# Kernel optimization log

Measured on AMD Instinct MI355X. Metric: run time of the kernel, lower is better.

Reference implementation:

```python
import jax, jax.numpy as jnp
import numpy as np

N_NODES = 256  # num_eeg_channels; reshape in head forces node count == channels

def setup_inputs() -> dict:
    key = jax.random.key(0)
    ks = jax.random.split(key, 16)
    T, H, L, E = 30000, 512, 256, 32768
    def w(k, shape):
        return jax.random.normal(k, shape, jnp.float32) / np.sqrt(shape[0]).astype(np.float32)
    return {
        "eeg_nodes": jax.random.normal(ks[0], (N_NODES, T), jnp.float32),
        "eeg_idx": jax.random.randint(ks[1], (2, E), 0, N_NODES),
        "eeg_attr": jax.random.uniform(ks[2], (E,), jnp.float32),
        # struct_featurizer GIN: conv1 MLP [T,H,H], conv2 MLP [H,L,L]
        "Ws1a": w(ks[3], (T, H)), "bs1a": jnp.zeros((H,), jnp.float32),
        "Ws1b": w(ks[4], (H, H)), "bs1b": jnp.zeros((H,), jnp.float32),
        "Ws2a": w(ks[5], (H, L)), "bs2a": jnp.zeros((L,), jnp.float32),
        "Ws2b": w(ks[6], (L, L)), "bs2b": jnp.zeros((L,), jnp.float32),
        # gin_scorer GIN: conv1 MLP [L,H,H], conv2 MLP [H,1,1]
        "Wc1a": w(ks[7], (L, H)), "bc1a": jnp.zeros((H,), jnp.float32),
        "Wc1b": w(ks[8], (H, H)), "bc1b": jnp.zeros((H,), jnp.float32),
        "Wc2a": w(ks[9], (H, 1)), "bc2a": jnp.zeros((1,), jnp.float32),
        "Wc2b": w(ks[10], (1, 1)), "bc2b": jnp.zeros((1,), jnp.float32),
        # dementia head: Linear(N*L, 1)
        "Wd": w(ks[11], (N_NODES * L, 1)), "bd": jnp.zeros((1,), jnp.float32),
    }


def _gin_conv(x, src, dst, W1, b1, W2, b2):
    # GINConv, eps=0: nn(x + sum_{j in N(i)} x_j); edge weights unsupported/ignored.
    agg = jax.ops.segment_sum(x[src], dst, num_segments=N_NODES)
    h = x + agg
    h = jax.nn.relu(h @ W1 + b1)  # MLP([in, out, out]) = Linear-ReLU-Linear
    return h @ W2 + b2


def reference(eeg_nodes, eeg_idx, eeg_attr,
              Ws1a, bs1a, Ws1b, bs1b, Ws2a, bs2a, Ws2b, bs2b,
              Wc1a, bc1a, Wc1b, bc1b, Wc2a, bc2a, Wc2b, bc2b,
              Wd, bd):
    src, dst = eeg_idx[0], eeg_idx[1]
    # struct_featurizer (2-layer GIN; inter-layer ReLU, edge_weight ignored by GINConv)
    h = _gin_conv(eeg_nodes, src, dst, Ws1a, bs1a, Ws1b, bs1b)
    h = jax.nn.relu(h)
    feat = _gin_conv(h, src, dst, Ws2a, bs2a, Ws2b, bs2b)  # [N, L]
    # gin_scorer (2-layer GIN)
    s = _gin_conv(feat, src, dst, Wc1a, bc1a, Wc1b, bc1b)
    s = jax.nn.relu(s)
    s = _gin_conv(s, src, dst, Wc2a, bc2a, Wc2b, bc2b)  # [N, 1]
    region_scores = jax.nn.sigmoid(s)
    flat = feat.reshape(1, -1)  # [1, N*L]
    dementia_pred = jax.nn.sigmoid(flat @ Wd + bd)  # [1, 1]
    return dementia_pred, region_scores
```

## Files before the change

### kernel.cpp

```cpp
#include <hip/hip_runtime.h>
#include <math.h>

#define N_NODES 256
#define T_DIM   30000
#define T_PAD   30016
#define H_DIM   512
#define L_DIM   256

typedef __attribute__((ext_vector_type(8))) short short8;
typedef __attribute__((ext_vector_type(4))) float floatx4;

__global__ void k_init_P(float* P, float* dem, float* u) {
    int t = blockIdx.x * blockDim.x + threadIdx.x;
    P[t] = ((t >> 8) == (t & 255)) ? 1.0f : 0.0f;
    if (t == 0) *dem = 0.0f;
    if (t < 256) u[t] = 0.0f;
}

__global__ void k_count_edges(const int* __restrict__ idx, int E, float* P) {
    int e = blockIdx.x * blockDim.x + threadIdx.x;
    if (e < E) {
        int s = idx[e];
        int d = idx[E + e];
        atomicAdd(&P[d * N_NODES + s], 1.0f);
    }
}

__global__ void k_zero(float* p, int n) {
    int t = blockIdx.x * blockDim.x + threadIdx.x;
    if (t < n) p[t] = 0.0f;
}

__device__ __forceinline__ unsigned short f2b(float f) {
    unsigned u = __float_as_uint(f);
    u += 0x7fffu + ((u >> 16) & 1u);
    return (unsigned short)(u >> 16);
}

__device__ __forceinline__ float4 zero4() {
    float4 z; z.x = z.y = z.z = z.w = 0.f; return z;
}

__global__ __launch_bounds__(256)
void k_gemm_mfma(const float* __restrict__ x, const float* __restrict__ W,
                 float* __restrict__ outp, int kc) {
    __shared__ unsigned short Al[128 * 40];
    __shared__ unsigned short Bl[128 * 40];

    const int t = threadIdx.x;
    const int orig = blockIdx.x;
    const int q = gridDim.x >> 3;
    const int L = (orig & 7) * q + (orig >> 3);
    const int tile = L & 7;
    const int colBase = (tile & 3) << 7;
    const int rowBase = (tile >> 2) << 7;
    const int z = L >> 3;
    const int kb0 = z * kc;
    const int kend = min(kb0 + kc, T_PAD);
    const int nchunk = (kend - kb0) >> 5;

    const int s_row  = t >> 1;
    const int s_half = (t & 1) << 4;
    const int s_k  = t & 31;
    const int s_cq = (t >> 5) << 4;

    const int w    = t >> 6;
    const int wr   = (w >> 1) << 6;
    const int wc   = (w & 1) << 6;
    const int lane = t & 63;
    const int lm   = lane & 15;
    const int lq   = (lane >> 4) << 3;

    floatx4 acc[4][4];
    #pragma unroll
    for (int i = 0; i < 4; ++i)
        #pragma unroll
        for (int j = 0; j < 4; ++j)
            acc[i][j] = (floatx4){0.f, 0.f, 0.f, 0.f};

    float4 pa[4], pb[4];
    {
        const int kg = kb0;
        const float* ap = x + (size_t)(rowBase + s_row) * T_DIM + kg + s_half;
        #pragma unroll
        for (int i = 0; i < 4; ++i)
            pa[i] = (kg + s_half + i * 4 + 4 <= T_DIM) ? *(const float4*)(ap + i * 4)
                                                       : zero4();
        const float* bp = W + (size_t)(kg + s_k) * H_DIM + colBase + s_cq;
        #pragma unroll
        for (int i = 0; i < 4; ++i)
            pb[i] = (kg + s_k < T_DIM) ? *(const float4*)(bp + i * 4) : zero4();
    }

    #pragma unroll 1
    for (int c = 0; c < nchunk; ++c) {
        __syncthreads();
        #pragma unroll
        for (int i = 0; i < 4; ++i) {
            ushort4 uv;
            uv.x = f2b(pa[i].x); uv.y = f2b(pa[i].y);
            uv.z = f2b(pa[i].z); uv.w = f2b(pa[i].w);
            *(ushort4*)&Al[s_row * 40 + s_half + i * 4] = uv;
        }
        #pragma unroll
        for (int i = 0; i < 4; ++i) {
            const int cb = s_cq + i * 4;
            Bl[(cb + 0) * 40 + s_k] = f2b(pb[i].x);
            Bl[(cb + 1) * 40 + s_k] = f2b(pb[i].y);
            Bl[(cb + 2) * 40 + s_k] = f2b(pb[i].z);
            Bl[(cb + 3) * 40 + s_k] = f2b(pb[i].w);
        }
        __syncthreads();

        if (c + 1 < nchunk) {
            const int kg = kb0 + (c + 1) * 32;
            const float* ap = x + (size_t)(rowBase + s_row) * T_DIM + kg + s_half;
            #pragma unroll
            for (int i = 0; i < 4; ++i)
                pa[i] = (kg + s_half + i * 4 + 4 <= T_DIM)
                            ? *(const float4*)(ap + i * 4) : zero4();
            const float* bp = W + (size_t)(kg + s_k) * H_DIM + colBase + s_cq;
            #pragma unroll
            for (int i = 0; i < 4; ++i)
                pb[i] = (kg + s_k < T_DIM) ? *(const float4*)(bp + i * 4) : zero4();
        }

        short8 af[4], bf[4];
        #pragma unroll
        for (int i = 0; i < 4; ++i)
            af[i] = *(const short8*)&Al[(wr + i * 16 + lm) * 40 + lq];
        #pragma unroll
        for (int j = 0; j < 4; ++j)
            bf[j] = *(const short8*)&Bl[(wc + j * 16 + lm) * 40 + lq];
        #pragma unroll
        for (int i = 0; i < 4; ++i)
            #pragma unroll
            for (int j = 0; j < 4; ++j)
                acc[i][j] = __builtin_amdgcn_mfma_f32_16x16x32_bf16(
                    af[i], bf[j], acc[i][j], 0, 0, 0);
    }

    float* op = outp + (size_t)z * (N_NODES * H_DIM);
    const int rq = (lane >> 4) << 2;
    #pragma unroll
    for (int i = 0; i < 4; ++i) {
        #pragma unroll
        for (int j = 0; j < 4; ++j) {
            const int r  = rowBase + wr + i * 16 + rq;
            const int cc = colBase + wc + j * 16 + lm;
            op[(size_t)(r + 0) * H_DIM + cc] = acc[i][j][0];
            op[(size_t)(r + 1) * H_DIM + cc] = acc[i][j][1];
            op[(size_t)(r + 2) * H_DIM + cc] = acc[i][j][2];
            op[(size_t)(r + 3) * H_DIM + cc] = acc[i][j][3];
        }
    }
}

__global__ __launch_bounds__(256)
void k_gemm_big_atomic(const float* __restrict__ x, const float* __restrict__ W,
                       float* __restrict__ outp, int kc) {
    __shared__ float xs[16 * 140];
    __shared__ float ws[16 * 132];
    const int t  = threadIdx.x;
    const int colBase = blockIdx.x * 128;
    const int rowBase = blockIdx.y * 128;
    const int kb0  = blockIdx.z * kc;
    const int kend = min(kb0 + kc, T_DIM);
    const int nchunk = (kend > kb0) ? ((kend - kb0) >> 4) : 0;
    const int lr  = t >> 2, lkq = (t & 3) * 4;
    const int wkk = t >> 5, wcq = (t & 31) * 4;
    const int tx  = t & 15, ty = t >> 4;
    float acc[8][8];
    #pragma unroll
    for (int i = 0; i < 8; ++i)
        #pragma unroll
        for (int j = 0; j < 8; ++j) acc[i][j] = 0.0f;
    #pragma unroll 1
    for (int c = 0; c < nchunk; ++c) {
        int kb = kb0 + c * 16;
        __syncthreads();
        const float* xp = x + (size_t)(rowBase + lr) * T_DIM + kb + lkq;
        float4 xa = *(const float4*)xp;
        float4 xb = *(const float4*)(xp + (size_t)64 * T_DIM);
        const float* wp = W + (size_t)(kb + wkk) * H_DIM + colBase + wcq;
        float4 wa = *(const float4*)wp;
        float4 wb = *(const float4*)(wp + 8 * H_DIM);
        xs[(lkq + 0) * 140 + lr] = xa.x; xs[(lkq + 1) * 140 + lr] = xa.y;
        xs[(lkq + 2) * 140 + lr] = xa.z; xs[(lkq + 3) * 140 + lr] = xa.w;
        xs[(lkq + 0) * 140 + lr + 64] = xb.x; xs[(lkq + 1) * 140 + lr + 64] = xb.y;
        xs[(lkq + 2) * 140 + lr + 64] = xb.z; xs[(lkq + 3) * 140 + lr + 64] = xb.w;
        *(float4*)&ws[wkk * 132 + wcq]       = wa;
        *(float4*)&ws[(wkk + 8) * 132 + wcq] = wb;
        __syncthreads();
        #pragma unroll
        for (int kk = 0; kk < 16; ++kk) {
            float a[8], b[8];
            *(float4*)&a[0] = *(const float4*)&xs[kk * 140 + ty * 8];
            *(float4*)&a[4] = *(const float4*)&xs[kk * 140 + ty * 8 + 4];
            *(float4*)&b[0] = *(const float4*)&ws[kk * 132 + tx * 8];
            *(float4*)&b[4] = *(const float4*)&ws[kk * 132 + tx * 8 + 4];
            #pragma unroll
            for (int i = 0; i < 8; ++i)
                #pragma unroll
                for (int j = 0; j < 8; ++j)
                    acc[i][j] = fmaf(a[i], b[j], acc[i][j]);
        }
    }
    if (nchunk == 0) return;
    #pragma unroll
    for (int i = 0; i < 8; ++i) {
        int r = rowBase + ty * 8 + i;
        #pragma unroll
        for (int j = 0; j < 8; ++j)
            atomicAdd(&outp[r * H_DIM + colBase + tx * 8 + j], acc[i][j]);
    }
}

__global__ void k_reduce(const float2* __restrict__ Y1p, float2* __restrict__ Y1,
                         int nz) {
    int i = blockIdx.x * blockDim.x + threadIdx.x;
    float2 s = Y1p[i];
    for (int z = 1; z < nz; ++z) {
        float2 v = Y1p[(size_t)z * 65536 + i];
        s.x += v.x; s.y += v.y;
    }
    Y1[i] = s;
}

template<int K, int N, int MODE>
__global__ __launch_bounds__(256)
void k_mstage(const float* __restrict__ A, const float* __restrict__ B,
              const float* __restrict__ bias, float* __restrict__ out, int act,
              const float* __restrict__ Wd, float* __restrict__ dem,
              const float* __restrict__ uW, float* __restrict__ u) {
    const int t = threadIdx.x;
    const int wv = (blockIdx.x << 2) | (t >> 6);
    const int nct = N >> 4;
    const int r0 = (wv / nct) << 4;
    const int c0 = (wv % nct) << 4;
    const int lane = t & 63;
    const int lm   = lane & 15;
    const int lq   = (lane >> 4) << 3;

    floatx4 accE = {0.f, 0.f, 0.f, 0.f};
    floatx4 accO = {0.f, 0.f, 0.f, 0.f};
    const float* ap = A + (size_t)(r0 + lm) * K + lq;
    const float* bp = B + (size_t)lq * N + c0 + lm;

    #pragma unroll 2
    for (int kb = 0; kb < K; kb += 64) {
        {
            float4 a0 = *(const float4*)(ap + kb);
            float4 a1 = *(const float4*)(ap + kb + 4);
            float b0 = bp[(size_t)(kb + 0) * N], b1 = bp[(size_t)(kb + 1) * N];
            float b2 = bp[(size_t)(kb + 2) * N], b3 = bp[(size_t)(kb + 3) * N];
            float b4 = bp[(size_t)(kb + 4) * N], b5 = bp[(size_t)(kb + 5) * N];
            float b6 = bp[(size_t)(kb + 6) * N], b7 = bp[(size_t)(kb + 7) * N];
            short8 af, bf;
            af[0] = (short)f2b(a0.x); af[1] = (short)f2b(a0.y);
            af[2] = (short)f2b(a0.z); af[3] = (short)f2b(a0.w);
            af[4] = (short)f2b(a1.x); af[5] = (short)f2b(a1.y);
            af[6] = (short)f2b(a1.z); af[7] = (short)f2b(a1.w);
            bf[0] = (short)f2b(b0); bf[1] = (short)f2b(b1);
            bf[2] = (short)f2b(b2); bf[3] = (short)f2b(b3);
            bf[4] = (short)f2b(b4); bf[5] = (short)f2b(b5);
            bf[6] = (short)f2b(b6); bf[7] = (short)f2b(b7);
            accE = __builtin_amdgcn_mfma_f32_16x16x32_bf16(af, bf, accE, 0, 0, 0);
        }
        {
            const int kc2 = kb + 32;
            float4 a0 = *(const float4*)(ap + kc2);
            float4 a1 = *(const float4*)(ap + kc2 + 4);
            float b0 = bp[(size_t)(kc2 + 0) * N], b1 = bp[(size_t)(kc2 + 1) * N];
            float b2 = bp[(size_t)(kc2 + 2) * N], b3 = bp[(size_t)(kc2 + 3) * N];
            float b4 = bp[(size_t)(kc2 + 4) * N], b5 = bp[(size_t)(kc2 + 5) * N];
            float b6 = bp[(size_t)(kc2 + 6) * N], b7 = bp[(size_t)(kc2 + 7) * N];
            short8 af, bf;
            af[0] = (short)f2b(a0.x); af[1] = (short)f2b(a0.y);
            af[2] = (short)f2b(a0.z); af[3] = (short)f2b(a0.w);
            af[4] = (short)f2b(a1.x); af[5] = (short)f2b(a1.y);
            af[6] = (short)f2b(a1.z); af[7] = (short)f2b(a1.w);
            bf[0] = (short)f2b(b0); bf[1] = (short)f2b(b1);
            bf[2] = (short)f2b(b2); bf[3] = (short)f2b(b3);
            bf[4] = (short)f2b(b4); bf[5] = (short)f2b(b5);
            bf[6] = (short)f2b(b6); bf[7] = (short)f2b(b7);
            accO = __builtin_amdgcn_mfma_f32_16x16x32_bf16(af, bf, accO, 0, 0, 0);
        }
    }

    const float bb = bias ? bias[c0 + lm] : 0.f;
    const int rq = (lane >> 4) << 2;
    float v[4];
    #pragma unroll
    for (int i = 0; i < 4; ++i) {
        v[i] = accE[i] + accO[i] + bb;
        if (act) v[i] = fmaxf(v[i], 0.f);
    }

    if (MODE == 2) {
        const float uw = uW[c0 + lm];
        #pragma unroll
        for (int i = 0; i < 4; ++i) {
            float p = v[i] * uw;
            #pragma unroll
            for (int off = 8; off; off >>= 1) p += __shfl_down(p, off, 16);
            if (lm == 0) atomicAdd(&u[r0 + rq + i], p);
        }
        return;
    }
    #pragma unroll
    for (int i = 0; i < 4; ++i)
        out[(size_t)(r0 + rq + i) * N + c0 + lm] = v[i];
    if (MODE == 1) {
        float p = 0.f;
        #pragma unroll
        for (int i = 0; i < 4; ++i)
            p += v[i] * Wd[(r0 + rq + i) * 256 + c0 + lm];
        #pragma unroll
        for (int off = 32; off; off >>= 1) p += __shfl_down(p, off, 64);
        if (lane == 0) atomicAdd(dem, p);
    }
}

__device__ __forceinline__ float sigmoidf(float x) {
    return 1.0f / (1.0f + expf(-x));
}

__global__ __launch_bounds__(256)
void k_final(const float* __restrict__ P, const float* __restrict__ u,
             const float* __restrict__ dem,
             const float* __restrict__ bc2a, const float* __restrict__ Wc2b,
             const float* __restrict__ bc2b, const float* __restrict__ bd,
             float* __restrict__ out) {
    __shared__ float red[4];
    const int b = blockIdx.x, t = threadIdx.x;
    float pv = P[b * 256 + t] * u[t];
    #pragma unroll
    for (int off = 32; off; off >>= 1) pv += __shfl_down(pv, off, 64);
    if ((t & 63) == 0) red[t >> 6] = pv;
    __syncthreads();
    if (t == 0) {
        float v = red[0] + red[1] + red[2] + red[3];
        float h2 = fmaxf(v + bc2a[0], 0.f);
        out[1 + b] = sigmoidf(h2 * Wc2b[0] + bc2b[0]);
        if (b == 0) out[0] = sigmoidf(*dem + bd[0]);
    }
}

extern "C" void kernel_launch(void* const* d_in, const int* in_sizes, int n_in,
                              void* d_out, int out_size, void* d_ws, size_t ws_size,
                              hipStream_t stream) {
    const float* x    = (const float*)d_in[0];
    const int*   idx  = (const int*)d_in[1];
    const float* Ws1a = (const float*)d_in[3];
    const float* bs1a = (const float*)d_in[4];
    const float* Ws1b = (const float*)d_in[5];
    const float* bs1b = (const float*)d_in[6];
    const float* Ws2a = (const float*)d_in[7];
    const float* bs2a = (const float*)d_in[8];
    const float* Ws2b = (const float*)d_in[9];
    const float* bs2b = (const float*)d_in[10];
    const float* Wc1a = (const float*)d_in[11];
    const float* bc1a = (const float*)d_in[12];
    const float* Wc1b = (const float*)d_in[13];
    const float* bc1b = (const float*)d_in[14];
    const float* Wc2a = (const float*)d_in[15];
    const float* bc2a = (const float*)d_in[16];
    const float* Wc2b = (const float*)d_in[17];
    const float* bc2b = (const float*)d_in[18];
    const float* Wd   = (const float*)d_in[19];
    const float* bd   = (const float*)d_in[20];
    float* out = (float*)d_out;
    const int E = in_sizes[1] / 2;

    float* w    = (float*)d_ws;
    float* P    = w;
    float* Y1   = P + 65536;
    float* bufA = Y1 + 131072;
    float* bufB = bufA + 131072;
    float* feat = bufB + 131072;
    float* u    = feat + 65536;
    float* dem  = u + 256;
    float* Y1p  = dem + 64;

    const long long fixed = (long long)(Y1p - w);
    const long long avail = (long long)(ws_size / 4) - fixed;
    int maxsplit = (avail > 0) ? (int)(avail / 131072) : 0;
    int nz = 0, kc = 0;
    const int CH32 = 938;
    if (maxsplit >= 2) {
        int splits = maxsplit < 56 ? maxsplit : 56;
        int cps = (CH32 + splits - 1) / splits;
        nz = (CH32 + cps - 1) / cps;
        kc = cps * 32;
    }

    k_init_P<<<256, 256, 0, stream>>>(P, dem, u);
    k_count_edges<<<(E + 255) / 256, 256, 0, stream>>>(idx, E, P);

    if (nz > 0) {
        k_gemm_mfma<<<8 * nz, 256, 0, stream>>>(x, Ws1a, Y1p, kc);
        k_reduce<<<256, 256, 0, stream>>>((const float2*)Y1p, (float2*)Y1, nz);
    } else {
        k_zero<<<512, 256, 0, stream>>>(Y1, N_NODES * H_DIM);
        k_gemm_big_atomic<<<dim3(4, 2, 63), 256, 0, stream>>>(x, Ws1a, Y1, 480);
    }

    k_mstage<256, 512, 0><<<128, 256, 0, stream>>>(P,    Y1,   bs1a, bufA, 1, 0, 0, 0, 0);
    k_mstage<512, 512, 0><<<128, 256, 0, stream>>>(bufA, Ws1b, bs1b, bufB, 1, 0, 0, 0, 0);
    k_mstage<256, 512, 0><<<128, 256, 0, stream>>>(P,    bufB, 0,    bufA, 0, 0, 0, 0, 0);
    k_mstage<512, 256, 0><<< 64, 256, 0, stream>>>(bufA, Ws2a, bs2a, bufB, 1, 0, 0, 0, 0);
    k_mstage<256, 256, 1><<< 64, 256, 0, stream>>>(bufB, Ws2b, bs2b, feat, 0, Wd, dem, 0, 0);
    k_mstage<256, 256, 0><<< 64, 256, 0, stream>>>(P,    feat, 0,    bufA, 0, 0, 0, 0, 0);
    k_mstage<256, 512, 0><<<128, 256, 0, stream>>>(bufA, Wc1a, bc1a, bufB, 1, 0, 0, 0, 0);
    k_mstage<512, 512, 2><<<128, 256, 0, stream>>>(bufB, Wc1b, bc1b, 0,    1, 0, 0, Wc2a, u);
    k_final<<<256, 256, 0, stream>>>(P, u, dem, bc2a, Wc2b, bc2b, bd, out);
}
```

Measured before the change: 267.7 us.

## Fuse post-GEMM stages into one cooperative kernel with grid syncs

Replaces the init, edge-count, reduce, eight matmul-stage and final launches with a single cooperative kernel of 512 one-wave blocks. Stages are separated by grid.sync instead of kernel boundaries, so per-launch overhead and idle gaps between small kernels go away. Stage code is moved into a shared device function with runtime K/N/MODE and no loop unrolling, which may cost some instruction efficiency. If the cooperative launch fails, the code falls back to the original multi-kernel sequence.

```diff
diff --git a/kernel.cpp b/kernel.cpp
--- a/kernel.cpp
+++ b/kernel.cpp
@@ -1,5 +1,8 @@
 #include <hip/hip_runtime.h>
+#include <hip/hip_cooperative_groups.h>
 #include <math.h>
+
+namespace cg = cooperative_groups;
 
 #define N_NODES 256
 #define T_DIM   30000
@@ -227,35 +230,31 @@
     Y1[i] = s;
 }
 
-template<int K, int N, int MODE>
-__global__ __launch_bounds__(256)
-void k_mstage(const float* __restrict__ A, const float* __restrict__ B,
-              const float* __restrict__ bias, float* __restrict__ out, int act,
-              const float* __restrict__ Wd, float* __restrict__ dem,
-              const float* __restrict__ uW, float* __restrict__ u) {
-    const int t = threadIdx.x;
-    const int wv = (blockIdx.x << 2) | (t >> 6);
+__device__ __forceinline__ void wave_stage(
+    int tile, int K, int N, int MODE,
+    const float* __restrict__ A, const float* __restrict__ B,
+    const float* __restrict__ bias, float* __restrict__ outp, int act,
+    const float* __restrict__ Wd, float* __restrict__ dem,
+    const float* __restrict__ uW, float* __restrict__ u, int lane) {
     const int nct = N >> 4;
-    const int r0 = (wv / nct) << 4;
-    const int c0 = (wv % nct) << 4;
-    const int lane = t & 63;
-    const int lm   = lane & 15;
-    const int lq   = (lane >> 4) << 3;
+    const int r0 = (tile / nct) << 4;
+    const int c0 = (tile % nct) << 4;
+    const int lm = lane & 15;
+    const int lq = (lane >> 4) << 3;
 
     floatx4 accE = {0.f, 0.f, 0.f, 0.f};
     floatx4 accO = {0.f, 0.f, 0.f, 0.f};
     const float* ap = A + (size_t)(r0 + lm) * K + lq;
     const float* bp = B + (size_t)lq * N + c0 + lm;
 
-    #pragma unroll 2
+    #pragma unroll 1
     for (int kb = 0; kb < K; kb += 64) {
         {
             float4 a0 = *(const float4*)(ap + kb);
             float4 a1 = *(const float4*)(ap + kb + 4);
-            float b0 = bp[(size_t)(kb + 0) * N], b1 = bp[(size_t)(kb + 1) * N];
-            float b2 = bp[(size_t)(kb + 2) * N], b3 = bp[(size_t)(kb + 3) * N];
-            float b4 = bp[(size_t)(kb + 4) * N], b5 = bp[(size_t)(kb + 5) * N];
-            float b6 = bp[(size_t)(kb + 6) * N], b7 = bp[(size_t)(kb + 7) * N];
+            const float* bq = bp + (size_t)kb * N;
+            float b0 = bq[0],     b1 = bq[(size_t)N],     b2 = bq[(size_t)2*N], b3 = bq[(size_t)3*N];
+            float b4 = bq[(size_t)4*N], b5 = bq[(size_t)5*N], b6 = bq[(size_t)6*N], b7 = bq[(size_t)7*N];
             short8 af, bf;
             af[0] = (short)f2b(a0.x); af[1] = (short)f2b(a0.y);
             af[2] = (short)f2b(a0.z); af[3] = (short)f2b(a0.w);
@@ -268,13 +267,12 @@
             accE = __builtin_amdgcn_mfma_f32_16x16x32_bf16(af, bf, accE, 0, 0, 0);
         }
         {
-            const int kc2 = kb + 32;
-            float4 a0 = *(const float4*)(ap + kc2);
-            float4 a1 = *(const float4*)(ap + kc2 + 4);
-            float b0 = bp[(size_t)(kc2 + 0) * N], b1 = bp[(size_t)(kc2 + 1) * N];
-            float b2 = bp[(size_t)(kc2 + 2) * N], b3 = bp[(size_t)(kc2 + 3) * N];
-            float b4 = bp[(size_t)(kc2 + 4) * N], b5 = bp[(size_t)(kc2 + 5) * N];
-            float b6 = bp[(size_t)(kc2 + 6) * N], b7 = bp[(size_t)(kc2 + 7) * N];
+            const int k2 = kb + 32;
+            float4 a0 = *(const float4*)(ap + k2);
+            float4 a1 = *(const float4*)(ap + k2 + 4);
+            const float* bq = bp + (size_t)k2 * N;
+            float b0 = bq[0],     b1 = bq[(size_t)N],     b2 = bq[(size_t)2*N], b3 = bq[(size_t)3*N];
+            float b4 = bq[(size_t)4*N], b5 = bq[(size_t)5*N], b6 = bq[(size_t)6*N], b7 = bq[(size_t)7*N];
             short8 af, bf;
             af[0] = (short)f2b(a0.x); af[1] = (short)f2b(a0.y);
             af[2] = (short)f2b(a0.z); af[3] = (short)f2b(a0.w);
@@ -310,7 +308,7 @@
     }
     #pragma unroll
     for (int i = 0; i < 4; ++i)
-        out[(size_t)(r0 + rq + i) * N + c0 + lm] = v[i];
+        outp[(size_t)(r0 + rq + i) * N + c0 + lm] = v[i];
     if (MODE == 1) {
         float p = 0.f;
         #pragma unroll
@@ -320,6 +318,17 @@
         for (int off = 32; off; off >>= 1) p += __shfl_down(p, off, 64);
         if (lane == 0) atomicAdd(dem, p);
     }
+}
+
+template<int K, int N, int MODE>
+__global__ __launch_bounds__(256)
+void k_mstage(const float* __restrict__ A, const float* __restrict__ B,
+              const float* __restrict__ bias, float* __restrict__ out, int act,
+              const float* __restrict__ Wd, float* __restrict__ dem,
+              const float* __restrict__ uW, float* __restrict__ u) {
+    const int t = threadIdx.x;
+    const int wv = (blockIdx.x << 2) | (t >> 6);
+    wave_stage(wv, K, N, MODE, A, B, bias, out, act, Wd, dem, uW, u, t & 63);
 }
 
 __device__ __forceinline__ float sigmoidf(float x) {
@@ -344,6 +353,84 @@
         float h2 = fmaxf(v + bc2a[0], 0.f);
         out[1 + b] = sigmoidf(h2 * Wc2b[0] + bc2b[0]);
         if (b == 0) out[0] = sigmoidf(*dem + bd[0]);
+    }
+}
+
+__global__ __launch_bounds__(64)
+void k_fused(const int* __restrict__ idx, int E, int nz,
+             const float* __restrict__ Y1p, float* __restrict__ Y1,
+             float* __restrict__ P,
+             const float* __restrict__ bs1a, const float* __restrict__ Ws1b,
+             const float* __restrict__ bs1b, const float* __restrict__ Ws2a,
+             const float* __restrict__ bs2a, const float* __restrict__ Ws2b,
+             const float* __restrict__ bs2b, const float* __restrict__ Wc1a,
+             const float* __restrict__ bc1a, const float* __restrict__ Wc1b,
+             const float* __restrict__ bc1b, const float* __restrict__ Wc2a,
+             const float* __restrict__ bc2a, const float* __restrict__ Wc2b,
+             const float* __restrict__ bc2b, const float* __restrict__ Wd,
+             const float* __restrict__ bd,
+             float* __restrict__ bufA, float* __restrict__ bufB,
+             float* __restrict__ feat, float* __restrict__ u,
+             float* __restrict__ dem, float* __restrict__ out) {
+    cg::grid_group grid = cg::this_grid();
+    const int b = blockIdx.x;
+    const int lane = threadIdx.x;
+    const int gid = (b << 6) | lane;
+
+    #pragma unroll
+    for (int i = gid; i < 65536; i += 32768)
+        P[i] = ((i >> 8) == (i & 255)) ? 1.0f : 0.0f;
+    if (nz > 0) {
+        const float4* src = (const float4*)Y1p;
+        float4 s = src[gid];
+        for (int z = 1; z < nz; ++z) {
+            float4 v = src[(size_t)z * 32768 + gid];
+            s.x += v.x; s.y += v.y; s.z += v.z; s.w += v.w;
+        }
+        ((float4*)Y1)[gid] = s;
+    }
+    if (gid < 256) u[gid] = 0.0f;
+    if (gid == 0) *dem = 0.0f;
+    grid.sync();
+
+    for (int e = gid; e < E; e += 32768) {
+        int s = idx[e];
+        int d = idx[E + e];
+        atomicAdd(&P[d * N_NODES + s], 1.0f);
+    }
+    grid.sync();
+
+    wave_stage(b, 256, 512, 0, P,    Y1,   bs1a, bufA, 1, 0, 0, 0, 0, lane);
+    grid.sync();
+    wave_stage(b, 512, 512, 0, bufA, Ws1b, bs1b, bufB, 1, 0, 0, 0, 0, lane);
+    grid.sync();
+    wave_stage(b, 256, 512, 0, P,    bufB, 0,    bufA, 0, 0, 0, 0, 0, lane);
+    grid.sync();
+    if (b < 256) wave_stage(b, 512, 256, 0, bufA, Ws2a, bs2a, bufB, 1, 0, 0, 0, 0, lane);
+    grid.sync();
+    if (b < 256) wave_stage(b, 256, 256, 1, bufB, Ws2b, bs2b, feat, 0, Wd, dem, 0, 0, lane);
+    grid.sync();
+    if (b < 256) wave_stage(b, 256, 256, 0, P,    feat, 0,    bufA, 0, 0, 0, 0, 0, lane);
+    grid.sync();
+    wave_stage(b, 256, 512, 0, bufA, Wc1a, bc1a, bufB, 1, 0, 0, 0, 0, lane);
+    grid.sync();
+    wave_stage(b, 512, 512, 2, bufB, Wc1b, bc1b, 0,    1, 0, 0, Wc2a, u, lane);
+    grid.sync();
+
+    if (b < 256) {
+        float pv = 0.f;
+        #pragma unroll
+        for (int j = 0; j < 4; ++j) {
+            int c = lane + 64 * j;
+            pv += P[b * 256 + c] * u[c];
+        }
+        #pragma unroll
+        for (int off = 32; off; off >>= 1) pv += __shfl_down(pv, off, 64);
+        if (lane == 0) {
+            float h2 = fmaxf(pv + bc2a[0], 0.f);
+            out[1 + b] = sigmoidf(h2 * Wc2b[0] + bc2b[0]);
+            if (b == 0) out[0] = sigmoidf(*dem + bd[0]);
+        }
     }
 }
 
@@ -371,7 +458,7 @@
     const float* Wd   = (const float*)d_in[19];
     const float* bd   = (const float*)d_in[20];
     float* out = (float*)d_out;
-    const int E = in_sizes[1] / 2;
+    int E = in_sizes[1] / 2;
 
     float* w    = (float*)d_ws;
     float* P    = w;
@@ -395,24 +482,36 @@
         kc = cps * 32;
     }
 
-    k_init_P<<<256, 256, 0, stream>>>(P, dem, u);
-    k_count_edges<<<(E + 255) / 256, 256, 0, stream>>>(idx, E, P);
-
     if (nz > 0) {
         k_gemm_mfma<<<8 * nz, 256, 0, stream>>>(x, Ws1a, Y1p, kc);
-        k_reduce<<<256, 256, 0, stream>>>((const float2*)Y1p, (float2*)Y1, nz);
     } else {
         k_zero<<<512, 256, 0, stream>>>(Y1, N_NODES * H_DIM);
         k_gemm_big_atomic<<<dim3(4, 2, 63), 256, 0, stream>>>(x, Ws1a, Y1, 480);
     }
 
-    k_mstage<256, 512, 0><<<128, 256, 0, stream>>>(P,    Y1,   bs1a, bufA, 1, 0, 0, 0, 0);
-    k_mstage<512, 512, 0><<<128, 256, 0, stream>>>(bufA, Ws1b, bs1b, bufB, 1, 0, 0, 0, 0);
-    k_mstage<256, 512, 0><<<128, 256, 0, stream>>>(P,    bufB, 0,    bufA, 0, 0, 0, 0, 0);
-    k_mstage<512, 256, 0><<< 64, 256, 0, stream>>>(bufA, Ws2a, bs2a, bufB, 1, 0, 0, 0, 0);
-    k_mstage<256, 256, 1><<< 64, 256, 0, stream>>>(bufB, Ws2b, bs2b, feat, 0, Wd, dem, 0, 0);
-    k_mstage<256, 256, 0><<< 64, 256, 0, stream>>>(P,    feat, 0,    bufA, 0, 0, 0, 0, 0);
-    k_mstage<256, 512, 0><<<128, 256, 0, stream>>>(bufA, Wc1a, bc1a, bufB, 1, 0, 0, 0, 0);
-    k_mstage<512, 512, 2><<<128, 256, 0, stream>>>(bufB, Wc1b, bc1b, 0,    1, 0, 0, Wc2a, u);
-    k_final<<<256, 256, 0, stream>>>(P, u, dem, bc2a, Wc2b, bc2b, bd, out);
-}
+    void* args[] = {
+        (void*)&idx, (void*)&E, (void*)&nz, (void*)&Y1p, (void*)&Y1, (void*)&P,
+        (void*)&bs1a, (void*)&Ws1b, (void*)&bs1b, (void*)&Ws2a, (void*)&bs2a,
+        (void*)&Ws2b, (void*)&bs2b, (void*)&Wc1a, (void*)&bc1a, (void*)&Wc1b,
+        (void*)&bc1b, (void*)&Wc2a, (void*)&bc2a, (void*)&Wc2b, (void*)&bc2b,
+        (void*)&Wd, (void*)&bd, (void*)&bufA, (void*)&bufB, (void*)&feat,
+        (void*)&u, (void*)&dem, (void*)&out
+    };
+    hipError_t ce = hipLaunchCooperativeKernel((const void*)k_fused, dim3(512),
+                                               dim3(64), args, 0, stream);
+    if (ce != hipSuccess) {
+        k_init_P<<<256, 256, 0, stream>>>(P, dem, u);
+        k_count_edges<<<(E + 255) / 256, 256, 0, stream>>>(idx, E, P);
+        if (nz > 0)
+            k_reduce<<<256, 256, 0, stream>>>((const float2*)Y1p, (float2*)Y1, nz);
+        k_mstage<256, 512, 0><<<128, 256, 0, stream>>>(P,    Y1,   bs1a, bufA, 1, 0, 0, 0, 0);
+        k_mstage<512, 512, 0><<<128, 256, 0, stream>>>(bufA, Ws1b, bs1b, bufB, 1, 0, 0, 0, 0);
+        k_mstage<256, 512, 0><<<128, 256, 0, stream>>>(P,    bufB, 0,    bufA, 0, 0, 0, 0, 0);
+        k_mstage<512, 256, 0><<< 64, 256, 0, stream>>>(bufA, Ws2a, bs2a, bufB, 1, 0, 0, 0, 0);
+        k_mstage<256, 256, 1><<< 64, 256, 0, stream>>>(bufB, Ws2b, bs2b, feat, 0, Wd, dem, 0, 0);
+        k_mstage<256, 256, 0><<< 64, 256, 0, stream>>>(P,    feat, 0,    bufA, 0, 0, 0, 0, 0);
+        k_mstage<256, 512, 0><<<128, 256, 0, stream>>>(bufA, Wc1a, bc1a, bufB, 1, 0, 0, 0, 0);
+        k_mstage<512, 512, 2><<<128, 256, 0, stream>>>(bufB, Wc1b, bc1b, 0,    1, 0, 0, Wc2a, u);
+        k_final<<<256, 256, 0, stream>>>(P, u, dem, bc2a, Wc2b, bc2b, bd, out);
+    }
+}
```

Result: slower. 798.6 us (+198.3%).

## Double-buffer global prefetch in big GEMM and fuse adjacency build into one kernel

Applied to the files above, without the earlier changes.

The main split-K MFMA GEMM now keeps two register sets of prefetched tiles and loads chunk c+2 while computing chunk c, which deepens the global-load pipeline to hide more latency at the cost of extra registers. Building the adjacency matrix now takes one kernel instead of init plus atomic edge counting: each block scans all edges and counts its own row in shared-memory atomics. This removes a launch and global atomics but makes each of the 256 blocks read the full edge list. The small MFMA stage gets a minor rewrite of its B-pointer arithmetic.

```diff
diff --git a/kernel.cpp b/kernel.cpp
--- a/kernel.cpp
+++ b/kernel.cpp
@@ -10,19 +10,21 @@
 typedef __attribute__((ext_vector_type(8))) short short8;
 typedef __attribute__((ext_vector_type(4))) float floatx4;
 
-__global__ void k_init_P(float* P, float* dem, float* u) {
-    int t = blockIdx.x * blockDim.x + threadIdx.x;
-    P[t] = ((t >> 8) == (t & 255)) ? 1.0f : 0.0f;
-    if (t == 0) *dem = 0.0f;
-    if (t < 256) u[t] = 0.0f;
-}
-
-__global__ void k_count_edges(const int* __restrict__ idx, int E, float* P) {
-    int e = blockIdx.x * blockDim.x + threadIdx.x;
-    if (e < E) {
-        int s = idx[e];
-        int d = idx[E + e];
-        atomicAdd(&P[d * N_NODES + s], 1.0f);
+__global__ __launch_bounds__(256)
+void k_buildP(const int* __restrict__ idx, int E, float* __restrict__ P,
+              float* __restrict__ dem, float* __restrict__ u) {
+    __shared__ float cnt[256];
+    const int row = blockIdx.x, t = threadIdx.x;
+    cnt[t] = 0.f;
+    __syncthreads();
+    for (int e = t; e < E; e += 256) {
+        if (idx[E + e] == row) atomicAdd(&cnt[idx[e]], 1.0f);
+    }
+    __syncthreads();
+    P[row * 256 + t] = cnt[t] + ((t == row) ? 1.0f : 0.0f);
+    if (row == 0) {
+        u[t] = 0.f;
+        if (t == 0) *dem = 0.f;
     }
 }
 
@@ -78,67 +80,66 @@
         for (int j = 0; j < 4; ++j)
             acc[i][j] = (floatx4){0.f, 0.f, 0.f, 0.f};
 
-    float4 pa[4], pb[4];
-    {
-        const int kg = kb0;
-        const float* ap = x + (size_t)(rowBase + s_row) * T_DIM + kg + s_half;
-        #pragma unroll
-        for (int i = 0; i < 4; ++i)
-            pa[i] = (kg + s_half + i * 4 + 4 <= T_DIM) ? *(const float4*)(ap + i * 4)
-                                                       : zero4();
-        const float* bp = W + (size_t)(kg + s_k) * H_DIM + colBase + s_cq;
-        #pragma unroll
-        for (int i = 0; i < 4; ++i)
-            pb[i] = (kg + s_k < T_DIM) ? *(const float4*)(bp + i * 4) : zero4();
-    }
+    float4 paA[4], pbA[4], paB[4], pbB[4];
+
+#define GLOAD(PA, PB, C) do {                                                  \
+        const int kg_ = kb0 + (C) * 32;                                        \
+        const float* ap_ = x + (size_t)(rowBase + s_row) * T_DIM + kg_ + s_half;\
+        _Pragma("unroll")                                                      \
+        for (int i_ = 0; i_ < 4; ++i_)                                         \
+            PA[i_] = (kg_ + s_half + i_ * 4 + 4 <= T_DIM)                      \
+                         ? *(const float4*)(ap_ + i_ * 4) : zero4();           \
+        const float* bp_ = W + (size_t)(kg_ + s_k) * H_DIM + colBase + s_cq;   \
+        _Pragma("unroll")                                                      \
+        for (int i_ = 0; i_ < 4; ++i_)                                         \
+            PB[i_] = (kg_ + s_k < T_DIM) ? *(const float4*)(bp_ + i_ * 4)      \
+                                         : zero4();                            \
+    } while (0)
+
+#define CHUNK_STEP(PA, PB, C) do {                                             \
+        __syncthreads();                                                       \
+        _Pragma("unroll")                                                      \
+        for (int i_ = 0; i_ < 4; ++i_) {                                       \
+            ushort4 uv_;                                                       \
+            uv_.x = f2b(PA[i_].x); uv_.y = f2b(PA[i_].y);                      \
+            uv_.z = f2b(PA[i_].z); uv_.w = f2b(PA[i_].w);                      \
+            *(ushort4*)&Al[s_row * 40 + s_half + i_ * 4] = uv_;                \
+        }                                                                      \
+        _Pragma("unroll")                                                      \
+        for (int i_ = 0; i_ < 4; ++i_) {                                       \
+            const int cb_ = s_cq + i_ * 4;                                     \
+            Bl[(cb_ + 0) * 40 + s_k] = f2b(PB[i_].x);                          \
+            Bl[(cb_ + 1) * 40 + s_k] = f2b(PB[i_].y);                          \
+            Bl[(cb_ + 2) * 40 + s_k] = f2b(PB[i_].z);                          \
+            Bl[(cb_ + 3) * 40 + s_k] = f2b(PB[i_].w);                          \
+        }                                                                      \
+        __syncthreads();                                                       \
+        if ((C) + 2 < nchunk) GLOAD(PA, PB, (C) + 2);                          \
+        short8 af_[4], bf_[4];                                                 \
+        _Pragma("unroll")                                                      \
+        for (int i_ = 0; i_ < 4; ++i_)                                         \
+            af_[i_] = *(const short8*)&Al[(wr + i_ * 16 + lm) * 40 + lq];      \
+        _Pragma("unroll")                                                      \
+        for (int j_ = 0; j_ < 4; ++j_)                                         \
+            bf_[j_] = *(const short8*)&Bl[(wc + j_ * 16 + lm) * 40 + lq];      \
+        _Pragma("unroll")                                                      \
+        for (int i_ = 0; i_ < 4; ++i_)                                         \
+            _Pragma("unroll")                                                  \
+            for (int j_ = 0; j_ < 4; ++j_)                                     \
+                acc[i_][j_] = __builtin_amdgcn_mfma_f32_16x16x32_bf16(         \
+                    af_[i_], bf_[j_], acc[i_][j_], 0, 0, 0);                   \
+    } while (0)
+
+    GLOAD(paA, pbA, 0);
+    if (nchunk > 1) GLOAD(paB, pbB, 1);
 
     #pragma unroll 1
-    for (int c = 0; c < nchunk; ++c) {
-        __syncthreads();
-        #pragma unroll
-        for (int i = 0; i < 4; ++i) {
-            ushort4 uv;
-            uv.x = f2b(pa[i].x); uv.y = f2b(pa[i].y);
-            uv.z = f2b(pa[i].z); uv.w = f2b(pa[i].w);
-            *(ushort4*)&Al[s_row * 40 + s_half + i * 4] = uv;
-        }
-        #pragma unroll
-        for (int i = 0; i < 4; ++i) {
-            const int cb = s_cq + i * 4;
-            Bl[(cb + 0) * 40 + s_k] = f2b(pb[i].x);
-            Bl[(cb + 1) * 40 + s_k] = f2b(pb[i].y);
-            Bl[(cb + 2) * 40 + s_k] = f2b(pb[i].z);
-            Bl[(cb + 3) * 40 + s_k] = f2b(pb[i].w);
-        }
-        __syncthreads();
-
-        if (c + 1 < nchunk) {
-            const int kg = kb0 + (c + 1) * 32;
-            const float* ap = x + (size_t)(rowBase + s_row) * T_DIM + kg + s_half;
-            #pragma unroll
-            for (int i = 0; i < 4; ++i)
-                pa[i] = (kg + s_half + i * 4 + 4 <= T_DIM)
-                            ? *(const float4*)(ap + i * 4) : zero4();
-            const float* bp = W + (size_t)(kg + s_k) * H_DIM + colBase + s_cq;
-            #pragma unroll
-            for (int i = 0; i < 4; ++i)
-                pb[i] = (kg + s_k < T_DIM) ? *(const float4*)(bp + i * 4) : zero4();
-        }
-
-        short8 af[4], bf[4];
-        #pragma unroll
-        for (int i = 0; i < 4; ++i)
-            af[i] = *(const short8*)&Al[(wr + i * 16 + lm) * 40 + lq];
-        #pragma unroll
-        for (int j = 0; j < 4; ++j)
-            bf[j] = *(const short8*)&Bl[(wc + j * 16 + lm) * 40 + lq];
-        #pragma unroll
-        for (int i = 0; i < 4; ++i)
-            #pragma unroll
-            for (int j = 0; j < 4; ++j)
-                acc[i][j] = __builtin_amdgcn_mfma_f32_16x16x32_bf16(
-                    af[i], bf[j], acc[i][j], 0, 0, 0);
-    }
+    for (int c = 0; c < nchunk; c += 2) {
+        CHUNK_STEP(paA, pbA, c);
+        if (c + 1 < nchunk) CHUNK_STEP(paB, pbB, c + 1);
+    }
+#undef GLOAD
+#undef CHUNK_STEP
 
     float* op = outp + (size_t)z * (N_NODES * H_DIM);
     const int rq = (lane >> 4) << 2;
@@ -252,10 +253,11 @@
         {
             float4 a0 = *(const float4*)(ap + kb);
             float4 a1 = *(const float4*)(ap + kb + 4);
-            float b0 = bp[(size_t)(kb + 0) * N], b1 = bp[(size_t)(kb + 1) * N];
-            float b2 = bp[(size_t)(kb + 2) * N], b3 = bp[(size_t)(kb + 3) * N];
-            float b4 = bp[(size_t)(kb + 4) * N], b5 = bp[(size_t)(kb + 5) * N];
-            float b6 = bp[(size_t)(kb + 6) * N], b7 = bp[(size_t)(kb + 7) * N];
+            const float* bq = bp + (size_t)kb * N;
+            float b0 = bq[0],           b1 = bq[(size_t)N];
+            float b2 = bq[(size_t)2*N], b3 = bq[(size_t)3*N];
+            float b4 = bq[(size_t)4*N], b5 = bq[(size_t)5*N];
+            float b6 = bq[(size_t)6*N], b7 = bq[(size_t)7*N];
             short8 af, bf;
             af[0] = (short)f2b(a0.x); af[1] = (short)f2b(a0.y);
             af[2] = (short)f2b(a0.z); af[3] = (short)f2b(a0.w);
@@ -268,13 +270,14 @@
             accE = __builtin_amdgcn_mfma_f32_16x16x32_bf16(af, bf, accE, 0, 0, 0);
         }
         {
-            const int kc2 = kb + 32;
-            float4 a0 = *(const float4*)(ap + kc2);
-            float4 a1 = *(const float4*)(ap + kc2 + 4);
-            float b0 = bp[(size_t)(kc2 + 0) * N], b1 = bp[(size_t)(kc2 + 1) * N];
-            float b2 = bp[(size_t)(kc2 + 2) * N], b3 = bp[(size_t)(kc2 + 3) * N];
-            float b4 = bp[(size_t)(kc2 + 4) * N], b5 = bp[(size_t)(kc2 + 5) * N];
-            float b6 = bp[(size_t)(kc2 + 6) * N], b7 = bp[(size_t)(kc2 + 7) * N];
+            const int k2 = kb + 32;
+            float4 a0 = *(const float4*)(ap + k2);
+            float4 a1 = *(const float4*)(ap + k2 + 4);
+            const float* bq = bp + (size_t)k2 * N;
+            float b0 = bq[0],           b1 = bq[(size_t)N];
+            float b2 = bq[(size_t)2*N], b3 = bq[(size_t)3*N];
+            float b4 = bq[(size_t)4*N], b5 = bq[(size_t)5*N];
+            float b6 = bq[(size_t)6*N], b7 = bq[(size_t)7*N];
             short8 af, bf;
             af[0] = (short)f2b(a0.x); af[1] = (short)f2b(a0.y);
             af[2] = (short)f2b(a0.z); af[3] = (short)f2b(a0.w);
@@ -395,8 +398,7 @@
         kc = cps * 32;
     }
 
-    k_init_P<<<256, 256, 0, stream>>>(P, dem, u);
-    k_count_edges<<<(E + 255) / 256, 256, 0, stream>>>(idx, E, P);
+    k_buildP<<<256, 256, 0, stream>>>(idx, E, P, dem, u);
 
     if (nz > 0) {
         k_gemm_mfma<<<8 * nz, 256, 0, stream>>>(x, Ws1a, Y1p, kc);
```

After: 316.0 us. +18.1%, slower.

## Pre-transpose Ws1a to bf16 and use swizzled 64-wide K tiles in big GEMM

Applied to the files above, without the earlier changes.

Adds a kernel that transposes the large Ws1a weight into a K-major bf16 buffer in workspace on every call. The main GEMM can then load B as contiguous 16-byte vectors instead of converting and scattering fp32 values into LDS element by element. The K chunk grows from 32 to 64 and LDS uses an XOR swizzle instead of padding to avoid bank conflicts. This costs an extra pass over the weight, more workspace (which can reduce the number of split-K slices), and more registers for the bigger prefetch.

```diff
diff --git a/kernel.cpp b/kernel.cpp
--- a/kernel.cpp
+++ b/kernel.cpp
@@ -3,7 +3,7 @@
 
 #define N_NODES 256
 #define T_DIM   30000
-#define T_PAD   30016
+#define KP      30016
 #define H_DIM   512
 #define L_DIM   256
 
@@ -42,10 +42,41 @@
 }
 
 __global__ __launch_bounds__(256)
-void k_gemm_mfma(const float* __restrict__ x, const float* __restrict__ W,
+void k_wt(const float* __restrict__ W, unsigned short* __restrict__ Wt) {
+    __shared__ float tile[64][65];
+    const int k0 = blockIdx.x << 6;
+    const int c0 = blockIdx.y << 6;
+    const int t  = threadIdx.x;
+    const int rr = t >> 4, c4 = (t & 15) << 2;
+    #pragma unroll
+    for (int i = 0; i < 4; ++i) {
+        const int k = k0 + rr + (i << 4);
+        float4 v = (k < T_DIM) ? *(const float4*)&W[(size_t)k * H_DIM + c0 + c4]
+                               : zero4();
+        tile[rr + (i << 4)][c4 + 0] = v.x;
+        tile[rr + (i << 4)][c4 + 1] = v.y;
+        tile[rr + (i << 4)][c4 + 2] = v.z;
+        tile[rr + (i << 4)][c4 + 3] = v.w;
+    }
+    __syncthreads();
+    const int cr = t >> 4, k4 = (t & 15) << 2;
+    #pragma unroll
+    for (int i = 0; i < 4; ++i) {
+        const int c = cr + (i << 4);
+        ushort4 o;
+        o.x = f2b(tile[k4 + 0][c]);
+        o.y = f2b(tile[k4 + 1][c]);
+        o.z = f2b(tile[k4 + 2][c]);
+        o.w = f2b(tile[k4 + 3][c]);
+        *(ushort4*)&Wt[(size_t)(c0 + c) * KP + k0 + k4] = o;
+    }
+}
+
+__global__ __launch_bounds__(256)
+void k_gemm_bf16(const float* __restrict__ x, const unsigned short* __restrict__ Wt,
                  float* __restrict__ outp, int kc) {
-    __shared__ unsigned short Al[128 * 40];
-    __shared__ unsigned short Bl[128 * 40];
+    __shared__ __align__(16) unsigned short Al[128 * 64];
+    __shared__ __align__(16) unsigned short Bl[128 * 64];
 
     const int t = threadIdx.x;
     const int orig = blockIdx.x;
@@ -56,13 +87,13 @@
     const int rowBase = (tile >> 2) << 7;
     const int z = L >> 3;
     const int kb0 = z * kc;
-    const int kend = min(kb0 + kc, T_PAD);
-    const int nchunk = (kend - kb0) >> 5;
-
-    const int s_row  = t >> 1;
-    const int s_half = (t & 1) << 4;
-    const int s_k  = t & 31;
-    const int s_cq = (t >> 5) << 4;
+    const int kend = min(kb0 + kc, KP);
+    const int nchunk = (kend - kb0) >> 6;
+
+    const int ar  = t >> 4, afc = t & 15;
+    const int br  = t >> 3, bhc = t & 7;
+    const float*          axp = x  + (size_t)(rowBase + ar) * T_DIM + afc * 4;
+    const unsigned short* bwp = Wt + (size_t)(colBase + br) * KP   + bhc * 8;
 
     const int w    = t >> 6;
     const int wr   = (w >> 1) << 6;
@@ -78,67 +109,69 @@
         for (int j = 0; j < 4; ++j)
             acc[i][j] = (floatx4){0.f, 0.f, 0.f, 0.f};
 
-    float4 pa[4], pb[4];
-    {
-        const int kg = kb0;
-        const float* ap = x + (size_t)(rowBase + s_row) * T_DIM + kg + s_half;
-        #pragma unroll
-        for (int i = 0; i < 4; ++i)
-            pa[i] = (kg + s_half + i * 4 + 4 <= T_DIM) ? *(const float4*)(ap + i * 4)
-                                                       : zero4();
-        const float* bp = W + (size_t)(kg + s_k) * H_DIM + colBase + s_cq;
-        #pragma unroll
-        for (int i = 0; i < 4; ++i)
-            pb[i] = (kg + s_k < T_DIM) ? *(const float4*)(bp + i * 4) : zero4();
-    }
+    float4 pa[8];
+    short8 pb[4];
+
+#define GLOAD(C) do {                                                          \
+        const int kg_ = kb0 + (C) * 64;                                        \
+        const int ke_ = kg_ + afc * 4;                                         \
+        _Pragma("unroll")                                                      \
+        for (int i_ = 0; i_ < 8; ++i_)                                         \
+            pa[i_] = (ke_ + 4 <= T_DIM)                                        \
+                         ? *(const float4*)(axp + (size_t)(16 * i_) * T_DIM + kg_) \
+                         : zero4();                                            \
+        _Pragma("unroll")                                                      \
+        for (int i_ = 0; i_ < 4; ++i_)                                         \
+            pb[i_] = *(const short8*)(bwp + (size_t)(32 * i_) * KP + kg_);     \
+    } while (0)
+
+    GLOAD(0);
 
     #pragma unroll 1
     for (int c = 0; c < nchunk; ++c) {
         __syncthreads();
         #pragma unroll
-        for (int i = 0; i < 4; ++i) {
+        for (int i = 0; i < 8; ++i) {
+            const int row = ar + 16 * i;
+            const int ga  = (afc >> 1) ^ (row & 7);
             ushort4 uv;
             uv.x = f2b(pa[i].x); uv.y = f2b(pa[i].y);
             uv.z = f2b(pa[i].z); uv.w = f2b(pa[i].w);
-            *(ushort4*)&Al[s_row * 40 + s_half + i * 4] = uv;
+            *(ushort4*)&Al[row * 64 + ga * 8 + (afc & 1) * 4] = uv;
         }
         #pragma unroll
         for (int i = 0; i < 4; ++i) {
-            const int cb = s_cq + i * 4;
-            Bl[(cb + 0) * 40 + s_k] = f2b(pb[i].x);
-            Bl[(cb + 1) * 40 + s_k] = f2b(pb[i].y);
-            Bl[(cb + 2) * 40 + s_k] = f2b(pb[i].z);
-            Bl[(cb + 3) * 40 + s_k] = f2b(pb[i].w);
+            const int row = br + 32 * i;
+            const int gb  = bhc ^ (row & 7);
+            *(short8*)&Bl[row * 64 + gb * 8] = pb[i];
         }
         __syncthreads();
 
-        if (c + 1 < nchunk) {
-            const int kg = kb0 + (c + 1) * 32;
-            const float* ap = x + (size_t)(rowBase + s_row) * T_DIM + kg + s_half;
+        if (c + 1 < nchunk) GLOAD(c + 1);
+
+        #pragma unroll
+        for (int s = 0; s < 2; ++s) {
+            const int gbase = (s << 2) | (lq >> 3);
+            short8 af[4], bf[4];
+            #pragma unroll
+            for (int i = 0; i < 4; ++i) {
+                const int R = wr + i * 16 + lm;
+                af[i] = *(const short8*)&Al[R * 64 + ((gbase ^ (R & 7)) << 3)];
+            }
+            #pragma unroll
+            for (int j = 0; j < 4; ++j) {
+                const int Cc = wc + j * 16 + lm;
+                bf[j] = *(const short8*)&Bl[Cc * 64 + ((gbase ^ (Cc & 7)) << 3)];
+            }
             #pragma unroll
             for (int i = 0; i < 4; ++i)
-                pa[i] = (kg + s_half + i * 4 + 4 <= T_DIM)
-                            ? *(const float4*)(ap + i * 4) : zero4();
-            const float* bp = W + (size_t)(kg + s_k) * H_DIM + colBase + s_cq;
-            #pragma unroll
-            for (int i = 0; i < 4; ++i)
-                pb[i] = (kg + s_k < T_DIM) ? *(const float4*)(bp + i * 4) : zero4();
-        }
-
-        short8 af[4], bf[4];
-        #pragma unroll
-        for (int i = 0; i < 4; ++i)
-            af[i] = *(const short8*)&Al[(wr + i * 16 + lm) * 40 + lq];
-        #pragma unroll
-        for (int j = 0; j < 4; ++j)
-            bf[j] = *(const short8*)&Bl[(wc + j * 16 + lm) * 40 + lq];
-        #pragma unroll
-        for (int i = 0; i < 4; ++i)
-            #pragma unroll
-            for (int j = 0; j < 4; ++j)
-                acc[i][j] = __builtin_amdgcn_mfma_f32_16x16x32_bf16(
-                    af[i], bf[j], acc[i][j], 0, 0, 0);
-    }
+                #pragma unroll
+                for (int j = 0; j < 4; ++j)
+                    acc[i][j] = __builtin_amdgcn_mfma_f32_16x16x32_bf16(
+                        af[i], bf[j], acc[i][j], 0, 0, 0);
+        }
+    }
+#undef GLOAD
 
     float* op = outp + (size_t)z * (N_NODES * H_DIM);
     const int rq = (lane >> 4) << 2;
@@ -252,10 +285,11 @@
         {
             float4 a0 = *(const float4*)(ap + kb);
             float4 a1 = *(const float4*)(ap + kb + 4);
-            float b0 = bp[(size_t)(kb + 0) * N], b1 = bp[(size_t)(kb + 1) * N];
-            float b2 = bp[(size_t)(kb + 2) * N], b3 = bp[(size_t)(kb + 3) * N];
-            float b4 = bp[(size_t)(kb + 4) * N], b5 = bp[(size_t)(kb + 5) * N];
-            float b6 = bp[(size_t)(kb + 6) * N], b7 = bp[(size_t)(kb + 7) * N];
+            const float* bq = bp + (size_t)kb * N;
+            float b0 = bq[0],           b1 = bq[(size_t)N];
+            float b2 = bq[(size_t)2*N], b3 = bq[(size_t)3*N];
+            float b4 = bq[(size_t)4*N], b5 = bq[(size_t)5*N];
+            float b6 = bq[(size_t)6*N], b7 = bq[(size_t)7*N];
             short8 af, bf;
             af[0] = (short)f2b(a0.x); af[1] = (short)f2b(a0.y);
             af[2] = (short)f2b(a0.z); af[3] = (short)f2b(a0.w);
@@ -268,13 +302,14 @@
             accE = __builtin_amdgcn_mfma_f32_16x16x32_bf16(af, bf, accE, 0, 0, 0);
         }
         {
-            const int kc2 = kb + 32;
-            float4 a0 = *(const float4*)(ap + kc2);
-            float4 a1 = *(const float4*)(ap + kc2 + 4);
-            float b0 = bp[(size_t)(kc2 + 0) * N], b1 = bp[(size_t)(kc2 + 1) * N];
-            float b2 = bp[(size_t)(kc2 + 2) * N], b3 = bp[(size_t)(kc2 + 3) * N];
-            float b4 = bp[(size_t)(kc2 + 4) * N], b5 = bp[(size_t)(kc2 + 5) * N];
-            float b6 = bp[(size_t)(kc2 + 6) * N], b7 = bp[(size_t)(kc2 + 7) * N];
+            const int k2 = kb + 32;
+            float4 a0 = *(const float4*)(ap + k2);
+            float4 a1 = *(const float4*)(ap + k2 + 4);
+            const float* bq = bp + (size_t)k2 * N;
+            float b0 = bq[0],           b1 = bq[(size_t)N];
+            float b2 = bq[(size_t)2*N], b3 = bq[(size_t)3*N];
+            float b4 = bq[(size_t)4*N], b5 = bq[(size_t)5*N];
+            float b6 = bq[(size_t)6*N], b7 = bq[(size_t)7*N];
             short8 af, bf;
             af[0] = (short)f2b(a0.x); af[1] = (short)f2b(a0.y);
             af[2] = (short)f2b(a0.z); af[3] = (short)f2b(a0.w);
@@ -381,25 +416,29 @@
     float* feat = bufB + 131072;
     float* u    = feat + 65536;
     float* dem  = u + 256;
-    float* Y1p  = dem + 64;
+    float* WtF  = dem + 64;
+    const size_t WT_F = ((size_t)H_DIM * KP) / 2;
+    float* Y1p  = WtF + WT_F;
+    unsigned short* Wt = (unsigned short*)WtF;
 
     const long long fixed = (long long)(Y1p - w);
     const long long avail = (long long)(ws_size / 4) - fixed;
     int maxsplit = (avail > 0) ? (int)(avail / 131072) : 0;
     int nz = 0, kc = 0;
-    const int CH32 = 938;
+    const int CH64 = 469;
     if (maxsplit >= 2) {
         int splits = maxsplit < 56 ? maxsplit : 56;
-        int cps = (CH32 + splits - 1) / splits;
-        nz = (CH32 + cps - 1) / cps;
-        kc = cps * 32;
+        int cps = (CH64 + splits - 1) / splits;
+        nz = (CH64 + cps - 1) / cps;
+        kc = cps * 64;
     }
 
     k_init_P<<<256, 256, 0, stream>>>(P, dem, u);
     k_count_edges<<<(E + 255) / 256, 256, 0, stream>>>(idx, E, P);
 
     if (nz > 0) {
-        k_gemm_mfma<<<8 * nz, 256, 0, stream>>>(x, Ws1a, Y1p, kc);
+        k_wt<<<dim3(469, 8), 256, 0, stream>>>(Ws1a, Wt);
+        k_gemm_bf16<<<8 * nz, 256, 0, stream>>>(x, Wt, Y1p, kc);
         k_reduce<<<256, 256, 0, stream>>>((const float2*)Y1p, (float2*)Y1, nz);
     } else {
         k_zero<<<512, 256, 0, stream>>>(Y1, N_NODES * H_DIM);
```

After: 260.8 us. 1.03x faster.
